# Optimization experiments

Hardware: AMD Instinct MI355X
Metric: run time of the kernel (lower is better)

The kernel has to match this reference:

```python
import jax, jax.numpy as jnp
import numpy as np

B, TQ, TK, H = 16, 128, 8192, 256

def setup_inputs() -> dict:
    key = jax.random.key(0)
    k1, k2 = jax.random.split(key)
    output_enc = jax.random.normal(k1, (B, TK, H), dtype=jnp.float32)
    hidden_dec = jax.random.normal(k2, (B, TQ, H), dtype=jnp.float32)
    return {"output_enc": output_enc, "hidden_dec": hidden_dec}

def reference(output_enc, hidden_dec):
    # scores: [B, TQ, TK] = hidden_dec @ output_enc^T (no 1/sqrt(H) scaling in original)
    scores = jnp.einsum('bqh,bkh->bqk', hidden_dec, output_enc)
    attn_weights = jax.nn.softmax(scores, axis=-1)
    # ctx: [B, TQ, H]
    ctx_vec = jnp.einsum('bqk,bkh->bqh', attn_weights, output_enc)
    return ctx_vec
```

## Files before the change

kernel.cpp:

```cpp
#include <hip/hip_runtime.h>
#include <hip/hip_bf16.h>


typedef _Float16 half8 __attribute__((ext_vector_type(8)));
typedef float floatx16 __attribute__((ext_vector_type(16)));
typedef unsigned int u32;

#define NB 16
#define TQ 128
#define TK 8192
#define HD 256
#define KSPLIT 16
#define KEYS_PER_SPLIT (TK / KSPLIT)
#define KB 32
#define NSUB (KEYS_PER_SPLIT / KB)


__global__ __launch_bounds__(512, 2) void attn_main(
    const float* __restrict__ enc, const float* __restrict__ dec,
    _Float16* __restrict__ pctx, float* __restrict__ pml) {
  __shared__ __align__(16) unsigned char smem[65536];
  const int tid = threadIdx.x;
  const int lane = tid & 63, wave = tid >> 6;
  const int wq = wave & 3;
  const int wh = wave >> 2;
  const int l31 = lane & 31, g2 = lane >> 5;
  const int b = blockIdx.x >> 4, ks = blockIdx.x & 15;

  half8 qf[16];
  {
    const float* qrow = dec + (size_t)(b * TQ + wq * 32 + l31) * HD;
#pragma unroll
    for (int c = 0; c < 16; ++c) {
      const float4* p4 = (const float4*)(qrow + c * 16 + g2 * 8);
      float4 x = p4[0], y = p4[1];
      half8 v;
      v[0] = (_Float16)x.x; v[1] = (_Float16)x.y; v[2] = (_Float16)x.z; v[3] = (_Float16)x.w;
      v[4] = (_Float16)y.x; v[5] = (_Float16)y.y; v[6] = (_Float16)y.z; v[7] = (_Float16)y.w;
      qf[c] = v;
    }
  }

  floatx16 ctx[4];
#pragma unroll
  for (int t = 0; t < 4; ++t)
#pragma unroll
    for (int i = 0; i < 16; ++i) ctx[t][i] = 0.f;
  float mrun = -1e30f, lrun = 0.f;

  const size_t keybase = (size_t)b * TK + (size_t)ks * KEYS_PER_SPLIT;

  const int sh0 = (tid & 63) * 4;
  const int sr0 = (tid >> 6) * 4;
  const int srv = (tid >> 6) >> 1;
  const int sa = (tid >> 6) & 1;

  float lv[4][4];

  auto LOAD = [&](int sc) {
#pragma unroll
    for (int j = 0; j < 4; ++j) {
      float4 t = *(const float4*)(enc + (keybase + (size_t)sc * KB + sr0 + j) * HD + sh0);
      lv[j][0] = t.x; lv[j][1] = t.y; lv[j][2] = t.z; lv[j][3] = t.w;
    }
  };

  auto WRITE = [&](int buf) {
    unsigned char* kb_ = smem + buf * 16384;
    unsigned char* vb_ = smem + 32768 + buf * 16384;
#pragma unroll
    for (int j = 0; j < 4; ++j) {
      int r = sr0 + j;
      u32 w0 = __builtin_bit_cast(u32, __builtin_amdgcn_cvt_pkrtz(lv[j][0], lv[j][1]));
      u32 w1 = __builtin_bit_cast(u32, __builtin_amdgcn_cvt_pkrtz(lv[j][2], lv[j][3]));
      *(uint2*)(kb_ + r * 512 + ((2 * sh0) ^ ((r & 7) << 4))) = make_uint2(w0, w1);
    }
#pragma unroll
    for (int u = 0; u < 4; ++u) {
      int h = sh0 + u;
      int slot = h ^ ((h >> 3) & 7) ^ srv;
      u32 w0 = __builtin_bit_cast(u32, __builtin_amdgcn_cvt_pkrtz(lv[0][u], lv[1][u]));
      u32 w1 = __builtin_bit_cast(u32, __builtin_amdgcn_cvt_pkrtz(lv[2][u], lv[3][u]));
      *(uint2*)(vb_ + srv * 4096 + slot * 16 + 8 * sa) = make_uint2(w0, w1);
    }
  };

  auto COMPUTE = [&](int buf) {
    const unsigned char* kb_ = smem + buf * 16384;
    const unsigned char* vb_ = smem + 32768 + buf * 16384;
    floatx16 S;
#pragma unroll
    for (int i = 0; i < 16; ++i) S[i] = 0.f;
    const int krow = l31 * 512;
    const int kx = (l31 & 7) << 4;
#pragma unroll
    for (int c = 0; c < 16; ++c) {
      half8 a = *(const half8*)(kb_ + krow + ((c * 32 + g2 * 16) ^ kx));
      S = __builtin_amdgcn_mfma_f32_32x32x16_f16(a, qf[c], S, 0, 0, 0);
    }
    float lmax = S[0];
#pragma unroll
    for (int i = 1; i < 16; ++i) lmax = fmaxf(lmax, S[i]);
    lmax = fmaxf(lmax, __shfl_xor(lmax, 32));
    if (__any(lmax > mrun + 8.f)) {
      float mn = fmaxf(mrun, lmax);
      float al = __expf(mrun - mn);
      lrun *= al;
      mrun = mn;
#pragma unroll
      for (int i = 0; i < 16; ++i) {
        int qn = (i & 3) + 8 * (i >> 2) + 4 * g2;
        float aq = __shfl(al, qn);
#pragma unroll
        for (int t = 0; t < 4; ++t) ctx[t][i] *= aq;
      }
    }
    float p[16];
    float rs = 0.f;
#pragma unroll
    for (int i = 0; i < 16; ++i) {
      p[i] = __expf(S[i] - mrun);
      rs += p[i];
    }
    rs += __shfl_xor(rs, 32);
    lrun += rs;
    u32 ph[8];
#pragma unroll
    for (int k2 = 0; k2 < 8; ++k2)
      ph[k2] = __builtin_bit_cast(u32, __builtin_amdgcn_cvt_pkrtz(p[2 * k2], p[2 * k2 + 1]));
#pragma unroll
    for (int c = 0; c < 2; ++c) {
      u32 a0 = ph[4 * c + 2 * g2], a1 = ph[4 * c + 2 * g2 + 1];
      u32 t0 = ph[4 * c + 2 * (1 - g2)], t1 = ph[4 * c + 2 * (1 - g2) + 1];
      u32 r0 = (u32)__shfl_xor((int)t0, 32);
      u32 r1 = (u32)__shfl_xor((int)t1, 32);
      union { u32 u[4]; half8 h8; } pf;
      if (g2 == 0) { pf.u[0] = a0; pf.u[1] = a1; pf.u[2] = r0; pf.u[3] = r1; }
      else         { pf.u[0] = r0; pf.u[1] = r1; pf.u[2] = a0; pf.u[3] = a1; }
      const int vrow = 2 * c + g2;
      const unsigned char* vr = vb_ + vrow * 4096;
#pragma unroll
      for (int ht = 0; ht < 4; ++ht) {
        int h = wh * 128 + ht * 32 + l31;
        int slot = h ^ ((h >> 3) & 7) ^ vrow;
        half8 vf = *(const half8*)(vr + slot * 16);
        ctx[ht] = __builtin_amdgcn_mfma_f32_32x32x16_f16(pf.h8, vf, ctx[ht], 0, 0, 0);
      }
    }
  };

  LOAD(0);
  WRITE(0);
  __syncthreads();
  for (int sc = 0; sc < NSUB; ++sc) {
    if (sc + 1 < NSUB) LOAD(sc + 1);
    COMPUTE(sc & 1);
    if (sc + 1 < NSUB) WRITE((sc + 1) & 1);
    __syncthreads();
  }

  float rl = 1.0f / lrun;
  float rlq[16];
#pragma unroll
  for (int i = 0; i < 16; ++i)
    rlq[i] = __shfl(rl, (i & 3) + 8 * (i >> 2) + 4 * g2);
  _Float16* base = pctx + (size_t)(ks * NB + b) * TQ * HD;
#pragma unroll
  for (int ht = 0; ht < 4; ++ht) {
    int h = wh * 128 + ht * 32 + l31;
#pragma unroll
    for (int i = 0; i < 16; ++i) {
      int qn = wq * 32 + (i & 3) + 8 * (i >> 2) + 4 * g2;
      base[(size_t)qn * HD + h] = (_Float16)(ctx[ht][i] * rlq[i]);
    }
  }
  if (wh == 0 && g2 == 0) {
    float* mp = pml + ((size_t)ks * (NB * TQ) + b * TQ + wq * 32 + l31) * 2;
    mp[0] = mrun;
    mp[1] = lrun;
  }
}

__global__ __launch_bounds__(256) void attn_combine(
    const _Float16* __restrict__ pctx, const float* __restrict__ pml,
    float* __restrict__ out) {
  const int bq = blockIdx.x;
  const int h = threadIdx.x;
  float mv[KSPLIT], lvv[KSPLIT];
  float M = -1e30f;
#pragma unroll
  for (int i = 0; i < KSPLIT; ++i) {
    const float* mp = pml + ((size_t)i * (NB * TQ) + bq) * 2;
    mv[i] = mp[0];
    lvv[i] = mp[1];
    M = fmaxf(M, mv[i]);
  }
  float ssum = 0.f, acc = 0.f;
#pragma unroll
  for (int i = 0; i < KSPLIT; ++i) {
    float w = lvv[i] * __expf(mv[i] - M);
    ssum += w;
    acc += w * (float)pctx[((size_t)i * (NB * TQ) + bq) * HD + h];
  }
  out[(size_t)bq * HD + h] = acc / ssum;
}

extern "C" void kernel_launch(void* const* d_in, const int* in_sizes, int n_in,
                              void* d_out, int out_size, void* d_ws, size_t ws_size,
                              hipStream_t stream) {
  const float* enc = (const float*)d_in[0];
  const float* dec = (const float*)d_in[1];
  float* out = (float*)d_out;
  _Float16* pctx = (_Float16*)d_ws;
  float* pml = (float*)((unsigned char*)d_ws +
                        (size_t)KSPLIT * NB * TQ * HD * sizeof(_Float16));
  hipLaunchKernelGGL(attn_main, dim3(NB * KSPLIT), dim3(512), 0, stream,
                     enc, dec, pctx, pml);
  hipLaunchKernelGGL(attn_combine, dim3(NB * TQ), dim3(256), 0, stream,
                     pctx, pml, out);
}
```

Baseline: 58.30 us.

## Double key splits, use 4-wave blocks covering full head dim, split-phase prefetch

Doubles KSPLIT to 32 and halves the block to 4 waves, each wave now owning 32 queries across all 256 head columns (8 ctx accumulators). This removes the duplicated QK^T work the old wh split caused. The global load and LDS write of the next tile is split into two halves interleaved with the QK and softmax/PV phases, and s_setprio is raised around the MFMA loops. Partial contexts are stored as packed fp16 pairs in a lane-contiguous layout, and combine is rewritten to decode that layout. The costs are higher register pressure, twice as much partial-result traffic, and more work in combine.

Result: slower. 146.9 us (+151.9%).

```diff
diff --git a/kernel.cpp b/kernel.cpp
--- a/kernel.cpp
+++ b/kernel.cpp
@@ -10,26 +10,24 @@
 #define TQ 128
 #define TK 8192
 #define HD 256
-#define KSPLIT 16
+#define KSPLIT 32
 #define KEYS_PER_SPLIT (TK / KSPLIT)
 #define KB 32
 #define NSUB (KEYS_PER_SPLIT / KB)
 
 
-__global__ __launch_bounds__(512, 2) void attn_main(
+__global__ __launch_bounds__(256, 2) void attn_main(
     const float* __restrict__ enc, const float* __restrict__ dec,
-    _Float16* __restrict__ pctx, float* __restrict__ pml) {
+    u32* __restrict__ pctx, float* __restrict__ pml) {
   __shared__ __align__(16) unsigned char smem[65536];
   const int tid = threadIdx.x;
   const int lane = tid & 63, wave = tid >> 6;
-  const int wq = wave & 3;
-  const int wh = wave >> 2;
   const int l31 = lane & 31, g2 = lane >> 5;
-  const int b = blockIdx.x >> 4, ks = blockIdx.x & 15;
+  const int b = blockIdx.x >> 5, ks = blockIdx.x & 31;
 
   half8 qf[16];
   {
-    const float* qrow = dec + (size_t)(b * TQ + wq * 32 + l31) * HD;
+    const float* qrow = dec + (size_t)(b * TQ + wave * 32 + l31) * HD;
 #pragma unroll
     for (int c = 0; c < 16; ++c) {
       const float4* p4 = (const float4*)(qrow + c * 16 + g2 * 8);
@@ -41,36 +39,35 @@
     }
   }
 
-  floatx16 ctx[4];
-#pragma unroll
-  for (int t = 0; t < 4; ++t)
+  floatx16 ctx[8];
+#pragma unroll
+  for (int t = 0; t < 8; ++t)
 #pragma unroll
     for (int i = 0; i < 16; ++i) ctx[t][i] = 0.f;
   float mrun = -1e30f, lrun = 0.f;
 
   const size_t keybase = (size_t)b * TK + (size_t)ks * KEYS_PER_SPLIT;
-
   const int sh0 = (tid & 63) * 4;
-  const int sr0 = (tid >> 6) * 4;
-  const int srv = (tid >> 6) >> 1;
-  const int sa = (tid >> 6) & 1;
-
-  float lv[4][4];
-
-  auto LOAD = [&](int sc) {
+  const int sr0 = (tid >> 6) * 8;
+  const int vrw = tid >> 6;
+
+  float la[4][4], lb[4][4];
+
+  auto LOADH = [&](int sc, int half, float (&lv)[4][4]) {
 #pragma unroll
     for (int j = 0; j < 4; ++j) {
-      float4 t = *(const float4*)(enc + (keybase + (size_t)sc * KB + sr0 + j) * HD + sh0);
+      float4 t = *(const float4*)(
+          enc + (keybase + (size_t)sc * KB + sr0 + half * 4 + j) * HD + sh0);
       lv[j][0] = t.x; lv[j][1] = t.y; lv[j][2] = t.z; lv[j][3] = t.w;
     }
   };
 
-  auto WRITE = [&](int buf) {
+  auto WRITEH = [&](int buf, int half, float (&lv)[4][4]) {
     unsigned char* kb_ = smem + buf * 16384;
     unsigned char* vb_ = smem + 32768 + buf * 16384;
 #pragma unroll
     for (int j = 0; j < 4; ++j) {
-      int r = sr0 + j;
+      int r = sr0 + half * 4 + j;
       u32 w0 = __builtin_bit_cast(u32, __builtin_amdgcn_cvt_pkrtz(lv[j][0], lv[j][1]));
       u32 w1 = __builtin_bit_cast(u32, __builtin_amdgcn_cvt_pkrtz(lv[j][2], lv[j][3]));
       *(uint2*)(kb_ + r * 512 + ((2 * sh0) ^ ((r & 7) << 4))) = make_uint2(w0, w1);
@@ -78,26 +75,32 @@
 #pragma unroll
     for (int u = 0; u < 4; ++u) {
       int h = sh0 + u;
-      int slot = h ^ ((h >> 3) & 7) ^ srv;
+      int slot = h ^ ((h >> 3) & 7) ^ vrw;
       u32 w0 = __builtin_bit_cast(u32, __builtin_amdgcn_cvt_pkrtz(lv[0][u], lv[1][u]));
       u32 w1 = __builtin_bit_cast(u32, __builtin_amdgcn_cvt_pkrtz(lv[2][u], lv[3][u]));
-      *(uint2*)(vb_ + srv * 4096 + slot * 16 + 8 * sa) = make_uint2(w0, w1);
-    }
-  };
-
-  auto COMPUTE = [&](int buf) {
+      *(uint2*)(vb_ + vrw * 4096 + slot * 16 + 8 * half) = make_uint2(w0, w1);
+    }
+  };
+
+  auto QK = [&](int buf) -> floatx16 {
     const unsigned char* kb_ = smem + buf * 16384;
-    const unsigned char* vb_ = smem + 32768 + buf * 16384;
     floatx16 S;
 #pragma unroll
     for (int i = 0; i < 16; ++i) S[i] = 0.f;
     const int krow = l31 * 512;
     const int kx = (l31 & 7) << 4;
+    __builtin_amdgcn_s_setprio(1);
 #pragma unroll
     for (int c = 0; c < 16; ++c) {
       half8 a = *(const half8*)(kb_ + krow + ((c * 32 + g2 * 16) ^ kx));
       S = __builtin_amdgcn_mfma_f32_32x32x16_f16(a, qf[c], S, 0, 0, 0);
     }
+    __builtin_amdgcn_s_setprio(0);
+    return S;
+  };
+
+  auto SMPV = [&](int buf, floatx16 S) {
+    const unsigned char* vb_ = smem + 32768 + buf * 16384;
     float lmax = S[0];
 #pragma unroll
     for (int i = 1; i < 16; ++i) lmax = fmaxf(lmax, S[i]);
@@ -112,7 +115,7 @@
         int qn = (i & 3) + 8 * (i >> 2) + 4 * g2;
         float aq = __shfl(al, qn);
 #pragma unroll
-        for (int t = 0; t < 4; ++t) ctx[t][i] *= aq;
+        for (int t = 0; t < 8; ++t) ctx[t][i] *= aq;
       }
     }
     float p[16];
@@ -139,23 +142,34 @@
       else         { pf.u[0] = r0; pf.u[1] = r1; pf.u[2] = a0; pf.u[3] = a1; }
       const int vrow = 2 * c + g2;
       const unsigned char* vr = vb_ + vrow * 4096;
-#pragma unroll
-      for (int ht = 0; ht < 4; ++ht) {
-        int h = wh * 128 + ht * 32 + l31;
+      __builtin_amdgcn_s_setprio(1);
+#pragma unroll
+      for (int ht = 0; ht < 8; ++ht) {
+        int h = ht * 32 + l31;
         int slot = h ^ ((h >> 3) & 7) ^ vrow;
         half8 vf = *(const half8*)(vr + slot * 16);
         ctx[ht] = __builtin_amdgcn_mfma_f32_32x32x16_f16(pf.h8, vf, ctx[ht], 0, 0, 0);
       }
-    }
-  };
-
-  LOAD(0);
-  WRITE(0);
+      __builtin_amdgcn_s_setprio(0);
+    }
+  };
+
+  LOADH(0, 0, la);
+  WRITEH(0, 0, la);
+  LOADH(0, 1, lb);
+  WRITEH(0, 1, lb);
   __syncthreads();
   for (int sc = 0; sc < NSUB; ++sc) {
-    if (sc + 1 < NSUB) LOAD(sc + 1);
-    COMPUTE(sc & 1);
-    if (sc + 1 < NSUB) WRITE((sc + 1) & 1);
+    const int cur = sc & 1, nxt = cur ^ 1;
+    const bool pfv = (sc + 1 < NSUB);
+    if (pfv) LOADH(sc + 1, 0, la);
+    floatx16 S = QK(cur);
+    if (pfv) {
+      WRITEH(nxt, 0, la);
+      LOADH(sc + 1, 1, lb);
+    }
+    SMPV(cur, S);
+    if (pfv) WRITEH(nxt, 1, lb);
     __syncthreads();
   }
 
@@ -164,43 +178,54 @@
 #pragma unroll
   for (int i = 0; i < 16; ++i)
     rlq[i] = __shfl(rl, (i & 3) + 8 * (i >> 2) + 4 * g2);
-  _Float16* base = pctx + (size_t)(ks * NB + b) * TQ * HD;
-#pragma unroll
-  for (int ht = 0; ht < 4; ++ht) {
-    int h = wh * 128 + ht * 32 + l31;
-#pragma unroll
-    for (int i = 0; i < 16; ++i) {
-      int qn = wq * 32 + (i & 3) + 8 * (i >> 2) + 4 * g2;
-      base[(size_t)qn * HD + h] = (_Float16)(ctx[ht][i] * rlq[i]);
-    }
-  }
-  if (wh == 0 && g2 == 0) {
-    float* mp = pml + ((size_t)ks * (NB * TQ) + b * TQ + wq * 32 + l31) * 2;
+  u32* pbase = pctx + (((size_t)(ks * NB + b) * 4 + wave) << 12);
+#pragma unroll
+  for (int ht = 0; ht < 8; ++ht)
+#pragma unroll
+    for (int j = 0; j < 8; ++j) {
+      float v0 = ctx[ht][2 * j] * rlq[2 * j];
+      float v1 = ctx[ht][2 * j + 1] * rlq[2 * j + 1];
+      pbase[(ht * 8 + j) * 64 + lane] =
+          __builtin_bit_cast(u32, __builtin_amdgcn_cvt_pkrtz(v0, v1));
+    }
+  if (g2 == 0) {
+    float* mp = pml + ((size_t)ks * (NB * TQ) + b * TQ + wave * 32 + l31) * 2;
     mp[0] = mrun;
     mp[1] = lrun;
   }
 }
 
 __global__ __launch_bounds__(256) void attn_combine(
-    const _Float16* __restrict__ pctx, const float* __restrict__ pml,
+    const u32* __restrict__ pctx, const float* __restrict__ pml,
     float* __restrict__ out) {
   const int bq = blockIdx.x;
+  const int b = bq >> 7, q = bq & 127;
   const int h = threadIdx.x;
+  const int wq = q >> 5, qn = q & 31;
+  const int g2 = (qn >> 2) & 1;
+  const int i = (qn & 3) + 4 * (qn >> 3);
+  const int j = i >> 1, b0 = i & 1;
+  const int ht = h >> 5;
+  const int ln = g2 * 32 + (h & 31);
+  const size_t boff = (((size_t)b * 4 + wq) << 12) + (ht * 8 + j) * 64 + ln;
+
   float mv[KSPLIT], lvv[KSPLIT];
   float M = -1e30f;
 #pragma unroll
-  for (int i = 0; i < KSPLIT; ++i) {
-    const float* mp = pml + ((size_t)i * (NB * TQ) + bq) * 2;
-    mv[i] = mp[0];
-    lvv[i] = mp[1];
-    M = fmaxf(M, mv[i]);
+  for (int s = 0; s < KSPLIT; ++s) {
+    const float* mp = pml + ((size_t)s * (NB * TQ) + bq) * 2;
+    mv[s] = mp[0];
+    lvv[s] = mp[1];
+    M = fmaxf(M, mv[s]);
   }
   float ssum = 0.f, acc = 0.f;
 #pragma unroll
-  for (int i = 0; i < KSPLIT; ++i) {
-    float w = lvv[i] * __expf(mv[i] - M);
+  for (int s = 0; s < KSPLIT; ++s) {
+    float w = lvv[s] * __expf(mv[s] - M);
     ssum += w;
-    acc += w * (float)pctx[((size_t)i * (NB * TQ) + bq) * HD + h];
+    union { u32 u; _Float16 hx[2]; } cv;
+    cv.u = pctx[(size_t)s * (NB * 4 * 4096) + boff];
+    acc += w * (float)cv.hx[b0];
   }
   out[(size_t)bq * HD + h] = acc / ssum;
 }
@@ -211,10 +236,10 @@
   const float* enc = (const float*)d_in[0];
   const float* dec = (const float*)d_in[1];
   float* out = (float*)d_out;
-  _Float16* pctx = (_Float16*)d_ws;
+  u32* pctx = (u32*)d_ws;
   float* pml = (float*)((unsigned char*)d_ws +
-                        (size_t)KSPLIT * NB * TQ * HD * sizeof(_Float16));
-  hipLaunchKernelGGL(attn_main, dim3(NB * KSPLIT), dim3(512), 0, stream,
+                        (size_t)KSPLIT * NB * 4 * 4096 * sizeof(u32));
+  hipLaunchKernelGGL(attn_main, dim3(NB * KSPLIT), dim3(256), 0, stream,
                      enc, dec, pctx, pml);
   hipLaunchKernelGGL(attn_combine, dim3(NB * TQ), dim3(256), 0, stream,
                      pctx, pml, out);
```

## Deepen global prefetch, relax barriers, prioritize MFMA, coalesce partial-context stores

Applied to the files above, without the earlier changes.

Encoder tiles are now prefetched two sub-chunks ahead, using two register staging buffers instead of one. `__syncthreads` is replaced by a barrier that waits only on LDS counters (`lgkmcnt`), so outstanding global loads stay in flight across iterations. The MFMA loops are wrapped in `s_setprio` raises to favour matrix issue. Partial context results are written as packed fp16 pairs in the MFMA fragment layout, giving coalesced 32-bit stores, and the combine kernel is remapped to read that layout. The extra 16 staging floats per thread raise register pressure under the 512x2 launch bound and may cause spills.

Measured after the change: 86.73 us. +48.8%, slower.

```diff
diff --git a/kernel.cpp b/kernel.cpp
--- a/kernel.cpp
+++ b/kernel.cpp
@@ -15,10 +15,12 @@
 #define KB 32
 #define NSUB (KEYS_PER_SPLIT / KB)
 
+#define BARRIER() asm volatile("s_waitcnt lgkmcnt(0)\n\ts_barrier" ::: "memory")
+
 
 __global__ __launch_bounds__(512, 2) void attn_main(
     const float* __restrict__ enc, const float* __restrict__ dec,
-    _Float16* __restrict__ pctx, float* __restrict__ pml) {
+    u32* __restrict__ pctx, float* __restrict__ pml) {
   __shared__ __align__(16) unsigned char smem[65536];
   const int tid = threadIdx.x;
   const int lane = tid & 63, wave = tid >> 6;
@@ -49,23 +51,23 @@
   float mrun = -1e30f, lrun = 0.f;
 
   const size_t keybase = (size_t)b * TK + (size_t)ks * KEYS_PER_SPLIT;
-
   const int sh0 = (tid & 63) * 4;
   const int sr0 = (tid >> 6) * 4;
   const int srv = (tid >> 6) >> 1;
   const int sa = (tid >> 6) & 1;
 
-  float lv[4][4];
-
-  auto LOAD = [&](int sc) {
+  float la[4][4], lb[4][4];
+
+  auto LOAD = [&](int sc, float (&lv)[4][4]) {
 #pragma unroll
     for (int j = 0; j < 4; ++j) {
-      float4 t = *(const float4*)(enc + (keybase + (size_t)sc * KB + sr0 + j) * HD + sh0);
+      float4 t = *(const float4*)(
+          enc + (keybase + (size_t)sc * KB + sr0 + j) * HD + sh0);
       lv[j][0] = t.x; lv[j][1] = t.y; lv[j][2] = t.z; lv[j][3] = t.w;
     }
   };
 
-  auto WRITE = [&](int buf) {
+  auto WRITE = [&](int buf, float (&lv)[4][4]) {
     unsigned char* kb_ = smem + buf * 16384;
     unsigned char* vb_ = smem + 32768 + buf * 16384;
 #pragma unroll
@@ -93,11 +95,13 @@
     for (int i = 0; i < 16; ++i) S[i] = 0.f;
     const int krow = l31 * 512;
     const int kx = (l31 & 7) << 4;
+    __builtin_amdgcn_s_setprio(1);
 #pragma unroll
     for (int c = 0; c < 16; ++c) {
       half8 a = *(const half8*)(kb_ + krow + ((c * 32 + g2 * 16) ^ kx));
       S = __builtin_amdgcn_mfma_f32_32x32x16_f16(a, qf[c], S, 0, 0, 0);
     }
+    __builtin_amdgcn_s_setprio(0);
     float lmax = S[0];
 #pragma unroll
     for (int i = 1; i < 16; ++i) lmax = fmaxf(lmax, S[i]);
@@ -115,19 +119,18 @@
         for (int t = 0; t < 4; ++t) ctx[t][i] *= aq;
       }
     }
-    float p[16];
     float rs = 0.f;
 #pragma unroll
     for (int i = 0; i < 16; ++i) {
-      p[i] = __expf(S[i] - mrun);
-      rs += p[i];
+      S[i] = __expf(S[i] - mrun);
+      rs += S[i];
     }
     rs += __shfl_xor(rs, 32);
     lrun += rs;
     u32 ph[8];
 #pragma unroll
     for (int k2 = 0; k2 < 8; ++k2)
-      ph[k2] = __builtin_bit_cast(u32, __builtin_amdgcn_cvt_pkrtz(p[2 * k2], p[2 * k2 + 1]));
+      ph[k2] = __builtin_bit_cast(u32, __builtin_amdgcn_cvt_pkrtz(S[2 * k2], S[2 * k2 + 1]));
 #pragma unroll
     for (int c = 0; c < 2; ++c) {
       u32 a0 = ph[4 * c + 2 * g2], a1 = ph[4 * c + 2 * g2 + 1];
@@ -139,6 +142,7 @@
       else         { pf.u[0] = r0; pf.u[1] = r1; pf.u[2] = a0; pf.u[3] = a1; }
       const int vrow = 2 * c + g2;
       const unsigned char* vr = vb_ + vrow * 4096;
+      __builtin_amdgcn_s_setprio(1);
 #pragma unroll
       for (int ht = 0; ht < 4; ++ht) {
         int h = wh * 128 + ht * 32 + l31;
@@ -146,17 +150,19 @@
         half8 vf = *(const half8*)(vr + slot * 16);
         ctx[ht] = __builtin_amdgcn_mfma_f32_32x32x16_f16(pf.h8, vf, ctx[ht], 0, 0, 0);
       }
+      __builtin_amdgcn_s_setprio(0);
     }
   };
 
-  LOAD(0);
-  WRITE(0);
-  __syncthreads();
+  LOAD(0, la);
+  LOAD(1, lb);
+  WRITE(0, la);
+  BARRIER();
   for (int sc = 0; sc < NSUB; ++sc) {
-    if (sc + 1 < NSUB) LOAD(sc + 1);
+    if (sc + 2 < NSUB) LOAD(sc + 2, (sc & 1) ? lb : la);
     COMPUTE(sc & 1);
-    if (sc + 1 < NSUB) WRITE((sc + 1) & 1);
-    __syncthreads();
+    if (sc + 1 < NSUB) WRITE((sc + 1) & 1, (sc & 1) ? la : lb);
+    BARRIER();
   }
 
   float rl = 1.0f / lrun;
@@ -164,16 +170,16 @@
 #pragma unroll
   for (int i = 0; i < 16; ++i)
     rlq[i] = __shfl(rl, (i & 3) + 8 * (i >> 2) + 4 * g2);
-  _Float16* base = pctx + (size_t)(ks * NB + b) * TQ * HD;
-#pragma unroll
-  for (int ht = 0; ht < 4; ++ht) {
-    int h = wh * 128 + ht * 32 + l31;
-#pragma unroll
-    for (int i = 0; i < 16; ++i) {
-      int qn = wq * 32 + (i & 3) + 8 * (i >> 2) + 4 * g2;
-      base[(size_t)qn * HD + h] = (_Float16)(ctx[ht][i] * rlq[i]);
-    }
-  }
+  u32* pbase = pctx + (size_t)(ks * NB + b) * 16384 + (wq * 2 + wh) * 2048;
+#pragma unroll
+  for (int ht = 0; ht < 4; ++ht)
+#pragma unroll
+    for (int j = 0; j < 8; ++j) {
+      float v0 = ctx[ht][2 * j] * rlq[2 * j];
+      float v1 = ctx[ht][2 * j + 1] * rlq[2 * j + 1];
+      pbase[(ht * 8 + j) * 64 + lane] =
+          __builtin_bit_cast(u32, __builtin_amdgcn_cvt_pkrtz(v0, v1));
+    }
   if (wh == 0 && g2 == 0) {
     float* mp = pml + ((size_t)ks * (NB * TQ) + b * TQ + wq * 32 + l31) * 2;
     mp[0] = mrun;
@@ -182,25 +188,36 @@
 }
 
 __global__ __launch_bounds__(256) void attn_combine(
-    const _Float16* __restrict__ pctx, const float* __restrict__ pml,
+    const u32* __restrict__ pctx, const float* __restrict__ pml,
     float* __restrict__ out) {
   const int bq = blockIdx.x;
+  const int b = bq >> 7, q = bq & 127;
   const int h = threadIdx.x;
+  const int wq = q >> 5, qn = q & 31;
+  const int g2 = (qn >> 2) & 1;
+  const int i = (qn & 3) + 4 * (qn >> 3);
+  const int j = i >> 1, b0 = i & 1;
+  const int wh = h >> 7, ht = (h >> 5) & 3;
+  const int ln = (h & 31) + 32 * g2;
+  const size_t boff = (size_t)b * 16384 + (wq * 2 + wh) * 2048 + (ht * 8 + j) * 64 + ln;
+
   float mv[KSPLIT], lvv[KSPLIT];
   float M = -1e30f;
 #pragma unroll
-  for (int i = 0; i < KSPLIT; ++i) {
-    const float* mp = pml + ((size_t)i * (NB * TQ) + bq) * 2;
-    mv[i] = mp[0];
-    lvv[i] = mp[1];
-    M = fmaxf(M, mv[i]);
+  for (int s = 0; s < KSPLIT; ++s) {
+    const float* mp = pml + ((size_t)s * (NB * TQ) + bq) * 2;
+    mv[s] = mp[0];
+    lvv[s] = mp[1];
+    M = fmaxf(M, mv[s]);
   }
   float ssum = 0.f, acc = 0.f;
 #pragma unroll
-  for (int i = 0; i < KSPLIT; ++i) {
-    float w = lvv[i] * __expf(mv[i] - M);
+  for (int s = 0; s < KSPLIT; ++s) {
+    float w = lvv[s] * __expf(mv[s] - M);
     ssum += w;
-    acc += w * (float)pctx[((size_t)i * (NB * TQ) + bq) * HD + h];
+    union { u32 u; _Float16 hx[2]; } cv;
+    cv.u = pctx[(size_t)s * (NB * 16384) + boff];
+    acc += w * (float)cv.hx[b0];
   }
   out[(size_t)bq * HD + h] = acc / ssum;
 }
@@ -211,9 +228,9 @@
   const float* enc = (const float*)d_in[0];
   const float* dec = (const float*)d_in[1];
   float* out = (float*)d_out;
-  _Float16* pctx = (_Float16*)d_ws;
+  u32* pctx = (u32*)d_ws;
   float* pml = (float*)((unsigned char*)d_ws +
-                        (size_t)KSPLIT * NB * TQ * HD * sizeof(_Float16));
+                        (size_t)KSPLIT * NB * 16384 * sizeof(u32));
   hipLaunchKernelGGL(attn_main, dim3(NB * KSPLIT), dim3(512), 0, stream,
                      enc, dec, pctx, pml);
   hipLaunchKernelGGL(attn_combine, dim3(NB * TQ), dim3(256), 0, stream,
```
